# Kernel tuning notes

Measured on AMD Instinct MI355X. Metric: run time of the kernel, lower is better.

## Reference

```python
import jax, jax.numpy as jnp
import numpy as np

D_MODEL = 512
D_IN = D_MODEL * 2          # inner Mamba2 d_model
D_STATE = 128
D_CONV = 4
EXPAND = 2
D_INNER = EXPAND * D_IN     # 2048
HEADDIM = 64
NHEADS = D_INNER // HEADDIM # 32
CONV_DIM = D_INNER + 2 * D_STATE          # x,B,C stream into depthwise conv
D_PROJ = 2 * D_INNER + 2 * D_STATE + NHEADS  # z, xBC, dt
BATCH, SEQ = 2, 4096


def setup_inputs() -> dict:
    key = jax.random.key(0)
    ks = jax.random.split(key, 32)
    r = lambda i, shape, s=1.0: jax.random.normal(ks[i], shape, jnp.float32) * s
    inp = {"x": r(0, (BATCH, SEQ, D_MODEL))}
    inp.update(
        pre_w=r(1, (D_MODEL, D_IN), 0.02), pre_b=jnp.zeros(D_IN, jnp.float32),
        pre_ln_g=jnp.ones(D_IN, jnp.float32), pre_ln_b=jnp.zeros(D_IN, jnp.float32),
        post_w=r(2, (D_IN, D_MODEL), 0.02), post_b=jnp.zeros(D_MODEL, jnp.float32),
        post_ln_g=jnp.ones(D_MODEL, jnp.float32), post_ln_b=jnp.zeros(D_MODEL, jnp.float32),
    )
    for j, m in enumerate(("f", "b")):
        o = 3 + j * 8
        inp[f"win_{m}"] = r(o, (D_IN, D_PROJ), 0.02)
        inp[f"convw_{m}"] = r(o + 1, (CONV_DIM, D_CONV), 0.2)
        inp[f"convb_{m}"] = jnp.zeros(CONV_DIM, jnp.float32)
        inp[f"dtb_{m}"] = r(o + 2, (NHEADS,), 0.1)
        inp[f"Alog_{m}"] = jnp.log(jnp.arange(1, NHEADS + 1, dtype=jnp.float32))
        inp[f"D_{m}"] = jnp.ones(NHEADS, jnp.float32)
        inp[f"normw_{m}"] = jnp.ones(D_INNER, jnp.float32)
        inp[f"wout_{m}"] = r(o + 3, (D_INNER, D_IN), 0.02)
    return inp


def layernorm(x, g, b, eps=1e-5):
    mu = x.mean(-1, keepdims=True)
    v = ((x - mu) ** 2).mean(-1, keepdims=True)
    return (x - mu) * jax.lax.rsqrt(v + eps) * g + b


def dwconv_causal(x, w, b):
    # x: [B,L,C], w: [C,K] depthwise causal conv
    xp = jnp.pad(x, ((0, 0), (D_CONV - 1, 0), (0, 0)))
    y = jax.lax.conv_general_dilated(xp.transpose(0, 2, 1), w[:, None, :], (1,), 'VALID',
                                     feature_group_count=w.shape[0])
    return y.transpose(0, 2, 1) + b


def mamba2(x, win, convw, convb, dtb, Alog, Dp, normw, wout):
    # x: [B,L,D_IN]  ->  [B,L,D_IN]
    zxbcdt = x @ win
    z, xBC, dt = jnp.split(zxbcdt, [D_INNER, D_INNER + CONV_DIM], axis=-1)
    dt = jax.nn.softplus(dt + dtb)                          # [B,L,H]
    xBC = jax.nn.silu(dwconv_causal(xBC, convw, convb))
    xs, Bm, Cm = jnp.split(xBC, [D_INNER, D_INNER + D_STATE], axis=-1)
    xs = xs.reshape(xs.shape[0], xs.shape[1], NHEADS, HEADDIM)  # [B,L,H,P]
    A = -jnp.exp(Alog)                                       # [H]
    decay = jnp.exp(dt * A)                                  # [B,L,H]

    def step(h, inp):
        x_t, B_t, C_t, dt_t, dec_t = inp                     # [B,H,P],[B,N],[B,N],[B,H],[B,H]
        h = h * dec_t[:, :, None, None] + (dt_t[:, :, None] * x_t)[..., None] * B_t[:, None, None, :]
        y_t = jnp.einsum('bhpn,bn->bhp', h, C_t)
        return h, y_t

    h0 = jnp.zeros((x.shape[0], NHEADS, HEADDIM, D_STATE), x.dtype)
    seq = (xs.transpose(1, 0, 2, 3), Bm.transpose(1, 0, 2), Cm.transpose(1, 0, 2),
           dt.transpose(1, 0, 2), decay.transpose(1, 0, 2))
    _, ys = jax.lax.scan(step, h0, seq)                      # ys: [L,B,H,P]
    y = ys.transpose(1, 0, 2, 3) + Dp[None, None, :, None] * xs
    y = y.reshape(y.shape[0], y.shape[1], D_INNER)
    # gated RMSNorm (norm_before_gate=False)
    yg = y * jax.nn.silu(z)
    yn = yg * jax.lax.rsqrt(jnp.mean(yg * yg, -1, keepdims=True) + 1e-5) * normw
    return yn @ wout


def nbimamba2(x, pre_w, pre_b, pre_ln_g, pre_ln_b, post_w, post_b, post_ln_g, post_ln_b,
              win_f, convw_f, convb_f, dtb_f, Alog_f, D_f, normw_f, wout_f,
              win_b, convw_b, convb_b, dtb_b, Alog_b, D_b, normw_b, wout_b):
    shortcut = x
    h = layernorm(x @ pre_w + pre_b, pre_ln_g, pre_ln_b)
    gate = jax.nn.silu(h)
    out_f = mamba2(h, win_f, convw_f, convb_f, dtb_f, Alog_f, D_f, normw_f, wout_f)
    out_b = jnp.flip(mamba2(jnp.flip(h, 1), win_b, convw_b, convb_b, dtb_b, Alog_b, D_b, normw_b, wout_b), 1)
    out = layernorm((out_f * gate + out_b * gate) @ post_w + post_b, post_ln_g, post_ln_b)
    return out + shortcut


def reference(x, pre_w, pre_b, pre_ln_g, pre_ln_b, post_w, post_b, post_ln_g, post_ln_b,
              win_f, convw_f, convb_f, dtb_f, Alog_f, D_f, normw_f, wout_f,
              win_b, convw_b, convb_b, dtb_b, Alog_b, D_b, normw_b, wout_b):
    return nbimamba2(x, pre_w, pre_b, pre_ln_g, pre_ln_b, post_w, post_b, post_ln_g, post_ln_b,
                     win_f, convw_f, convb_f, dtb_f, Alog_f, D_f, normw_f, wout_f,
                     win_b, convw_b, convb_b, dtb_b, Alog_b, D_b, normw_b, wout_b)
```

## Files before the change

### kernel.cpp

```cpp
#include <hip/hip_runtime.h>
#include <stdint.h>

typedef unsigned short u16;
typedef __attribute__((ext_vector_type(8))) short short8;
typedef __attribute__((ext_vector_type(4))) float f32x4;

__device__ __forceinline__ float bf2f(u16 u) {
  union { float f; uint32_t i; } v; v.i = ((uint32_t)u) << 16; return v.f;
}
__device__ __forceinline__ u16 f2bf(float f) {
  union { float f; uint32_t i; } v; v.f = f;
  uint32_t r = v.i + 0x7FFFu + ((v.i >> 16) & 1u);
  return (u16)(r >> 16);
}
__device__ __forceinline__ uint32_t pk2(float a, float b) {
  return (uint32_t)f2bf(a) | ((uint32_t)f2bf(b) << 16);
}
__device__ __forceinline__ void gload16(const u16* g, u16* l) {
  __builtin_amdgcn_global_load_lds(
      (const __attribute__((address_space(1))) unsigned int*)g,
      (__attribute__((address_space(3))) unsigned int*)l, 16, 0, 0);
}

__device__ __forceinline__ float block_sum256(float v) {
  __shared__ float red[4];
  #pragma unroll
  for (int o = 1; o < 64; o <<= 1) v += __shfl_xor(v, o, 64);
  int lane = threadIdx.x & 63, w = threadIdx.x >> 6;
  __syncthreads();
  if (lane == 0) red[w] = v;
  __syncthreads();
  return red[0] + red[1] + red[2] + red[3];
}

__global__ void k_tcast(const float* __restrict__ W, u16* __restrict__ Wt,
                        int K, int N, int Npad) {
  __shared__ float tile[32][33];
  int n0 = blockIdx.x * 32, k0 = blockIdx.y * 32;
  int tx = threadIdx.x, ty0 = threadIdx.y;
  #pragma unroll
  for (int i = 0; i < 4; i++) {
    int ty = ty0 + i * 8;
    int k = k0 + ty, n = n0 + tx;
    tile[ty][tx] = (k < K && n < N) ? W[(size_t)k * N + n] : 0.f;
  }
  __syncthreads();
  #pragma unroll
  for (int i = 0; i < 4; i++) {
    int ty = ty0 + i * 8;
    int n = n0 + ty, k = k0 + tx;
    if (n < Npad && k < K) Wt[(size_t)n * K + k] = f2bf(tile[tx][ty]);
  }
}

__global__ void k_cast(const float* __restrict__ in, u16* __restrict__ out, int n4) {
  int i = blockIdx.x * 256 + threadIdx.x;
  if (i >= n4) return;
  float4 v = ((const float4*)in)[i];
  uint2 o;
  o.x = pk2(v.x, v.y);
  o.y = pk2(v.z, v.w);
  ((uint2*)out)[i] = o;
}

__launch_bounds__(256)
__global__ void k_gemm(const u16* __restrict__ A, const u16* __restrict__ Bt,
                       float* __restrict__ Cf, u16* __restrict__ Cb,
                       int M, int N, int K, int ldc, int flags) {
  __shared__ u16 lA[2][128 * 64];
  __shared__ u16 lB[2][128 * 64];
  const int tid = threadIdx.x;
  const int lane = tid & 63;
  const int wave = tid >> 6;
  const int bm = blockIdx.x, bn = blockIdx.y;
  const int wr = wave >> 1, wc = wave & 1;
  const int fr = lane & 15, fq = lane >> 4;

  const int srow = wave * 32 + (lane >> 3);
  const int scol = ((lane & 7) ^ (srow & 7)) * 8;
  const u16* gA = A + (size_t)(bm * 128 + srow) * K + scol;
  const u16* gB = Bt + (size_t)(bn * 128 + srow) * K + scol;
  const int lofs = wave * 2048;

  f32x4 acc[4][4] = {};

  #pragma unroll
  for (int i = 0; i < 4; i++) {
    gload16(gA + (size_t)(i * 8) * K, &lA[0][lofs + i * 512]);
    gload16(gB + (size_t)(i * 8) * K, &lB[0][lofs + i * 512]);
  }
  __syncthreads();

  const int NT = K >> 6;
  for (int t = 0; t < NT; ++t) {
    const int cur = t & 1;
    if (t + 1 < NT) {
      const int kt = (t + 1) << 6;
      #pragma unroll
      for (int i = 0; i < 4; i++) {
        gload16(gA + (size_t)(i * 8) * K + kt, &lA[cur ^ 1][lofs + i * 512]);
        gload16(gB + (size_t)(i * 8) * K + kt, &lB[cur ^ 1][lofs + i * 512]);
      }
    }
    #pragma unroll
    for (int kk = 0; kk < 2; kk++) {
      short8 af[4], bfr[4];
      #pragma unroll
      for (int m = 0; m < 4; m++) {
        int row = wr * 64 + m * 16 + fr;
        int sl = (kk * 4 + fq) ^ (row & 7);
        af[m] = *(const short8*)(&lA[cur][row * 64 + sl * 8]);
      }
      #pragma unroll
      for (int n = 0; n < 4; n++) {
        int row = wc * 64 + n * 16 + fr;
        int sl = (kk * 4 + fq) ^ (row & 7);
        bfr[n] = *(const short8*)(&lB[cur][row * 64 + sl * 8]);
      }
      #pragma unroll
      for (int m = 0; m < 4; m++)
        #pragma unroll
        for (int n = 0; n < 4; n++)
          acc[m][n] = __builtin_amdgcn_mfma_f32_16x16x32_bf16(af[m], bfr[n], acc[m][n], 0, 0, 0);
    }
    __syncthreads();
  }

  const bool bf16out = flags & 1, accum = flags & 2, flip = flags & 4;
  #pragma unroll
  for (int m = 0; m < 4; m++) {
    #pragma unroll
    for (int q = 0; q < 4; q++) {
      int rr = bm * 128 + wr * 64 + m * 16 + fq * 4 + q;
      int orow = flip ? (rr ^ 4095) : rr;
      size_t rb = (size_t)orow * ldc;
      #pragma unroll
      for (int n = 0; n < 4; n++) {
        int cc = bn * 128 + wc * 64 + n * 16 + fr;
        float v = acc[m][n][q];
        if (accum) v += Cf[rb + cc];
        if (bf16out) Cb[rb + cc] = f2bf(v);
        else Cf[rb + cc] = v;
      }
    }
  }
}

__global__ void k_preln(const float* __restrict__ t, const float* __restrict__ bias,
                        const float* __restrict__ g, const float* __restrict__ bb,
                        u16* __restrict__ out) {
  const int row = blockIdx.x, tid = threadIdx.x;
  float4 v = ((const float4*)(t + (size_t)row * 1024))[tid];
  float4 bi = ((const float4*)bias)[tid];
  float v0 = v.x + bi.x, v1 = v.y + bi.y, v2 = v.z + bi.z, v3 = v.w + bi.w;
  float mean = block_sum256(v0 + v1 + v2 + v3) * (1.f / 1024.f);
  float d0 = v0 - mean, d1 = v1 - mean, d2 = v2 - mean, d3 = v3 - mean;
  float var = block_sum256(d0 * d0 + d1 * d1 + d2 * d2 + d3 * d3) * (1.f / 1024.f);
  float rs = rsqrtf(var + 1e-5f);
  float4 gg = ((const float4*)g)[tid];
  float4 bv = ((const float4*)bb)[tid];
  uint2 o;
  o.x = pk2(d0 * rs * gg.x + bv.x, d1 * rs * gg.y + bv.y);
  o.y = pk2(d2 * rs * gg.z + bv.z, d3 * rs * gg.w + bv.w);
  ((uint2*)(out + (size_t)row * 1024))[tid] = o;
}

__global__ void k_dt2(const u16* __restrict__ zx, const float* __restrict__ dtb,
                      const float* __restrict__ Alog, float* __restrict__ DTt,
                      float* __restrict__ DECt, int flip) {
  int t = blockIdx.x * 256 + threadIdx.x;
  int h = blockIdx.y, b = blockIdx.z;
  int ts = flip ? 4095 - t : t;
  float raw = bf2f(zx[(size_t)((b << 12) + ts) * 4480 + 4352 + h]) + dtb[h];
  float d = (raw > 20.f) ? raw : log1pf(__expf(raw));
  size_t o = (size_t)(b * 32 + h) * 4096 + t;
  DTt[o] = d;
  DECt[o] = __expf(-__expf(Alog[h]) * d);
}

__global__ void k_conv2(const u16* __restrict__ zx, const float* __restrict__ cw,
                        const float* __restrict__ cb, u16* __restrict__ XT,
                        u16* __restrict__ BCtok, u16* __restrict__ BCT, int flip) {
  const int ct = blockIdx.x;
  const int tt = blockIdx.y;
  const int b = blockIdx.z;
  const int tid = threadIdx.x;
  __shared__ float sin_[67][64];
  __shared__ float sout[64][65];
  const int ch0 = ct * 64, t0 = tt * 64;

  for (int i = tid; i < 67 * 64; i += 256) {
    int r = i >> 6, ch = i & 63;
    int tok = t0 - 3 + r;
    float v = 0.f;
    if (tok >= 0) {
      int src = (b << 12) + (flip ? 4095 - tok : tok);
      v = bf2f(zx[(size_t)src * 4480 + 2048 + ch0 + ch]);
    }
    sin_[r][ch] = v;
  }
  __syncthreads();

  const int ch = tid & 63, g = tid >> 6;
  const int chg = ch0 + ch;
  float4 wv = *(const float4*)(cw + (size_t)chg * 4);
  float bias = cb[chg];
  #pragma unroll
  for (int i = 0; i < 16; i++) {
    int tl = g * 16 + i;
    float a = bias + wv.x * sin_[tl][ch] + wv.y * sin_[tl + 1][ch]
                   + wv.z * sin_[tl + 2][ch] + wv.w * sin_[tl + 3][ch];
    sout[tl][ch] = a / (1.f + __expf(-a));
  }
  __syncthreads();

  if (ch0 < 2048) {
    #pragma unroll
    for (int k = 0; k < 16; k++) {
      int chw = g + k * 4;
      int tl = tid & 63;
      XT[((size_t)(b * 2048 + ch0 + chw)) * 4096 + t0 + tl] = f2bf(sout[tl][chw]);
    }
  } else {
    int c2b = (ct - 32) * 64;
    #pragma unroll
    for (int k = 0; k < 16; k++) {
      int chw = g + k * 4;
      int tl = tid & 63;
      BCT[((size_t)(b * 256 + c2b + chw)) * 4096 + t0 + tl] = f2bf(sout[tl][chw]);
    }
    #pragma unroll
    for (int k = 0; k < 16; k++) {
      int r = g + k * 4;
      BCtok[((size_t)(b * 4096 + t0 + r)) * 256 + c2b + ch] = f2bf(sout[r][ch]);
    }
  }
}

#define NCH 16
#define SWZ(row, oct, msk) (((oct) ^ ((row) & (msk))) << 4)

__device__ __forceinline__ void cumsum256(int tid, int lane, float adt, float dtv,
                                          float* sL, float* sdt, float* spart) {
  float v = adt;
  if (tid < 256) {
    #pragma unroll
    for (int o = 1; o < 64; o <<= 1) {
      float t = __shfl_up(v, o, 64);
      if (lane >= o) v += t;
    }
    if (lane == 63) spart[tid >> 6] = v;
  }
  __syncthreads();
  if (tid < 256) {
    int w = tid >> 6;
    float off = 0.f;
    #pragma unroll
    for (int j = 0; j < 3; j++) if (j < w) off += spart[j];
    sL[tid] = v + off;
    sdt[tid] = dtv;
  }
}

__launch_bounds__(512, 1)
__global__ void k_ssd_a(const u16* __restrict__ XT, const u16* __restrict__ BCT,
                        const float* __restrict__ DTt, const float* __restrict__ Alog,
                        float* __restrict__ HB, float* __restrict__ PR) {
  const int c = blockIdx.x, h = blockIdx.y, b = blockIdx.z;
  const int tid = threadIdx.x;
  const int lane = tid & 63, w = tid >> 6;
  const int fr = lane & 15, fq = lane >> 4;
  const int bh = b * 32 + h;

  __shared__ u16 sX[64 * 256];
  __shared__ u16 sBW[128 * 256];
  __shared__ float sL[256], sdt[256], sw_[256], spart[4];

  float dtv = 0.f;
  if (tid < 256) dtv = DTt[(size_t)bh * 4096 + c * 256 + tid];
  float expA = __expf(Alog[h]);
  cumsum256(tid, lane, -expA * dtv, dtv, sL, sdt, spart);
  __syncthreads();
  if (tid < 256) sw_[tid] = __expf(sL[255] - sL[tid]) * sdt[tid];
  for (int i = tid; i < 2048; i += 512) {
    int p = i >> 5, oct = i & 31;
    uint4 v = *(const uint4*)(XT + ((size_t)(b * 2048 + h * 64 + p) << 12) + c * 256 + oct * 8);
    *(uint4*)((char*)sX + p * 512 + SWZ(p, oct, 15)) = v;
  }
  __syncthreads();
  for (int i = tid; i < 4096; i += 512) {
    int n = i >> 5, oct = i & 31;
    uint4 v = *(const uint4*)(BCT + ((size_t)(b * 256 + n) << 12) + c * 256 + oct * 8);
    const float* swp = sw_ + oct * 8;
    float f0 = bf2f((u16)(v.x & 0xFFFF)) * swp[0];
    float f1 = bf2f((u16)(v.x >> 16)) * swp[1];
    float f2 = bf2f((u16)(v.y & 0xFFFF)) * swp[2];
    float f3 = bf2f((u16)(v.y >> 16)) * swp[3];
    float f4 = bf2f((u16)(v.z & 0xFFFF)) * swp[4];
    float f5 = bf2f((u16)(v.z >> 16)) * swp[5];
    float f6 = bf2f((u16)(v.w & 0xFFFF)) * swp[6];
    float f7 = bf2f((u16)(v.w >> 16)) * swp[7];
    uint4 o;
    o.x = pk2(f0, f1); o.y = pk2(f2, f3); o.z = pk2(f4, f5); o.w = pk2(f6, f7);
    *(uint4*)((char*)sBW + n * 512 + SWZ(n, oct, 15)) = o;
  }
  __syncthreads();

  const int pb = w >> 1, nh = w & 1;
  f32x4 acc[4] = {};
  #pragma unroll
  for (int ks = 0; ks < 8; ks++) {
    int p = pb * 16 + fr;
    short8 af = *(const short8*)((char*)sX + p * 512 + SWZ(p, ks * 4 + fq, 15));
    #pragma unroll
    for (int nb = 0; nb < 4; nb++) {
      int n = nh * 64 + nb * 16 + fr;
      short8 bfm = *(const short8*)((char*)sBW + n * 512 + SWZ(n, ks * 4 + fq, 15));
      acc[nb] = __builtin_amdgcn_mfma_f32_16x16x32_bf16(af, bfm, acc[nb], 0, 0, 0);
    }
  }
  float* hb = HB + (size_t)(bh * NCH + c) * 8192;
  #pragma unroll
  for (int nb = 0; nb < 4; nb++)
    #pragma unroll
    for (int q = 0; q < 4; q++) {
      int p = pb * 16 + fq * 4 + q;
      int n = nh * 64 + nb * 16 + fr;
      hb[p * 128 + n] = acc[nb][q];
    }
  if (tid == 0) PR[bh * NCH + c] = __expf(sL[255]);
}

__global__ void k_scan_b(float* __restrict__ HB, const float* __restrict__ PR) {
  const int eb = blockIdx.x, h = blockIdx.y, b = blockIdx.z;
  const int e = eb * 256 + threadIdx.x;
  const int bh = b * 32 + h;
  float* base = HB + (size_t)bh * NCH * 8192 + e;
  const float* pr = PR + bh * NCH;
  float carry = 0.f;
  #pragma unroll 4
  for (int c = 0; c < NCH; ++c) {
    float v = base[(size_t)c * 8192];
    base[(size_t)c * 8192] = carry;
    carry = pr[c] * carry + v;
  }
}

__launch_bounds__(512, 1)
__global__ void k_ssd_c(const u16* __restrict__ BCtok, const u16* __restrict__ XT,
                        const float* __restrict__ DTt, const float* __restrict__ HB,
                        const float* __restrict__ Alog, const float* __restrict__ Dp,
                        u16* __restrict__ Y) {
  const int c = blockIdx.x, h = blockIdx.y, b = blockIdx.z;
  const int tid = threadIdx.x;
  const int lane = tid & 63, w = tid >> 6;
  const int fr = lane & 15, fq = lane >> 4;
  const int bh = b * 32 + h;
  const size_t m0 = (size_t)b * 4096 + c * 256;

  __shared__ u16 sB[256 * 128];
  __shared__ u16 sX[64 * 256];
  __shared__ u16 sH[64 * 128];
  __shared__ u16 sP[8 * 32 * 64];
  __shared__ float sL[256], sdt[256], spart[4];

  float dtv = 0.f;
  if (tid < 256) dtv = DTt[(size_t)bh * 4096 + c * 256 + tid];
  float expA = __expf(Alog[h]);
  cumsum256(tid, lane, -expA * dtv, dtv, sL, sdt, spart);

  for (int i = tid; i < 4096; i += 512) {
    int tr = i >> 4, oct = i & 15;
    uint4 v = *(const uint4*)(BCtok + ((m0 + tr) << 8) + oct * 8);
    *(uint4*)((char*)sB + tr * 256 + SWZ(tr, oct, 15)) = v;
  }
  for (int i = tid; i < 2048; i += 512) {
    int p = i >> 5, oct = i & 31;
    uint4 v = *(const uint4*)(XT + ((size_t)(b * 2048 + h * 64 + p) << 12) + c * 256 + oct * 8);
    *(uint4*)((char*)sX + p * 512 + SWZ(p, oct, 15)) = v;
  }
  for (int i = tid; i < 1024; i += 512) {
    int p = i >> 4, oct = i & 15;
    const float* src = HB + (size_t)(bh * NCH + c) * 8192 + p * 128 + oct * 8;
    float4 a = *(const float4*)src;
    float4 bb4 = *(const float4*)(src + 4);
    uint4 o;
    o.x = pk2(a.x, a.y); o.y = pk2(a.z, a.w); o.z = pk2(bb4.x, bb4.y); o.w = pk2(bb4.z, bb4.w);
    *(uint4*)((char*)sH + p * 256 + SWZ(p, oct, 15)) = o;
  }
  short8 cf[2][4];
  #pragma unroll
  for (int m = 0; m < 2; m++)
    #pragma unroll
    for (int ks = 0; ks < 4; ks++)
      cf[m][ks] = *(const short8*)(BCtok + ((m0 + w * 32 + m * 16 + fr) << 8) + 128 + ks * 32 + fq * 8);
  __syncthreads();

  float Lt[2][4], eLt[2][4];
  #pragma unroll
  for (int m = 0; m < 2; m++)
    #pragma unroll
    for (int q = 0; q < 4; q++) {
      Lt[m][q] = sL[w * 32 + m * 16 + fq * 4 + q];
      eLt[m][q] = __expf(Lt[m][q]);
    }
  const float Dh = Dp[h];

  f32x4 accY[2][4] = {};
  u16* pw = sP + w * 2048;
  const int ntl = (w >> 1) + 1;
  for (int tt = 0; tt < ntl; tt++) {
    const int t0 = tt * 64;
    f32x4 g[2][4] = {};
    #pragma unroll
    for (int ks = 0; ks < 4; ks++) {
      short8 bfm[4];
      #pragma unroll
      for (int nb = 0; nb < 4; nb++) {
        int tr = t0 + nb * 16 + fr;
        bfm[nb] = *(const short8*)((char*)sB + tr * 256 + SWZ(tr, ks * 4 + fq, 15));
      }
      #pragma unroll
      for (int m = 0; m < 2; m++)
        #pragma unroll
        for (int nb = 0; nb < 4; nb++)
          g[m][nb] = __builtin_amdgcn_mfma_f32_16x16x32_bf16(cf[m][ks], bfm[nb], g[m][nb], 0, 0, 0);
    }
    #pragma unroll
    for (int nb = 0; nb < 4; nb++) {
      int tau = t0 + nb * 16 + fr;
      float Ltau = sL[tau], dtau = sdt[tau];
      #pragma unroll
      for (int m = 0; m < 2; m++) {
        #pragma unroll
        for (int q = 0; q < 4; q++) {
          int t = w * 32 + m * 16 + fq * 4 + q;
          float mask = (tau > t) ? 0.f : __expf(Lt[m][q] - Ltau) * dtau;
          float pv = mask * g[m][nb][q];
          pv = (tau == t) ? pv + Dh : pv;
          int tl = m * 16 + fq * 4 + q, taul = nb * 16 + fr;
          *(u16*)((char*)pw + tl * 128 + ((((taul) >> 3) ^ (tl & 7)) << 4) + (taul & 7) * 2) = f2bf(pv);
        }
      }
    }
    #pragma unroll
    for (int ks = 0; ks < 2; ks++) {
      short8 pf[2], xf[4];
      #pragma unroll
      for (int m = 0; m < 2; m++) {
        int tl = m * 16 + fr;
        pf[m] = *(const short8*)((char*)pw + tl * 128 + (((ks * 4 + fq) ^ (tl & 7)) << 4));
      }
      #pragma unroll
      for (int pb = 0; pb < 4; pb++) {
        int p = pb * 16 + fr;
        int oct = (t0 >> 3) + ks * 4 + fq;
        xf[pb] = *(const short8*)((char*)sX + p * 512 + SWZ(p, oct, 15));
      }
      #pragma unroll
      for (int m = 0; m < 2; m++)
        #pragma unroll
        for (int pb = 0; pb < 4; pb++)
          accY[m][pb] = __builtin_amdgcn_mfma_f32_16x16x32_bf16(pf[m], xf[pb], accY[m][pb], 0, 0, 0);
    }
  }
  f32x4 accO[2][4] = {};
  #pragma unroll
  for (int ks = 0; ks < 4; ks++) {
    short8 hf[4];
    #pragma unroll
    for (int pb = 0; pb < 4; pb++) {
      int p = pb * 16 + fr;
      hf[pb] = *(const short8*)((char*)sH + p * 256 + SWZ(p, ks * 4 + fq, 15));
    }
    #pragma unroll
    for (int m = 0; m < 2; m++)
      #pragma unroll
      for (int pb = 0; pb < 4; pb++)
        accO[m][pb] = __builtin_amdgcn_mfma_f32_16x16x32_bf16(cf[m][ks], hf[pb], accO[m][pb], 0, 0, 0);
  }
  #pragma unroll
  for (int m = 0; m < 2; m++)
    #pragma unroll
    for (int pb = 0; pb < 4; pb++)
      #pragma unroll
      for (int q = 0; q < 4; q++) {
        int t = w * 32 + m * 16 + fq * 4 + q;
        float val = accY[m][pb][q] + eLt[m][q] * accO[m][pb][q];
        Y[(m0 + t) * 2048 + h * 64 + pb * 16 + fr] = f2bf(val);
      }
}

__launch_bounds__(256)
__global__ void k_scan(const u16* __restrict__ XT, const u16* __restrict__ BCtok,
                       const float* __restrict__ DTt, const float* __restrict__ DECt,
                       const float* __restrict__ Dp, u16* __restrict__ y) {
  const int ps = blockIdx.x, h = blockIdx.y, b = blockIdx.z;
  const int tid = threadIdx.x;
  const int tsub = tid & 15, pl = tid >> 4;
  const int p = ps * 16 + pl;
  const u16* xp = XT + ((size_t)(b * 2048 + h * 64 + p)) * 4096;
  const float* dth = DTt + (size_t)(b * 32 + h) * 4096;
  const float* dch = DECt + (size_t)(b * 32 + h) * 4096;
  u16* yp = y + (size_t)b * 4096 * 2048 + h * 64 + p;
  const float Dh = Dp[h];
  float s0 = 0, s1 = 0, s2 = 0, s3 = 0, s4 = 0, s5 = 0, s6 = 0, s7 = 0;
  for (int tau = 0; tau < 4096; ++tau) {
    const u16* bcr = BCtok + ((size_t)(b * 4096 + tau)) * 256;
    uint4 vB = *(const uint4*)(bcr + tsub * 8);
    uint4 vC = *(const uint4*)(bcr + 128 + tsub * 8);
    float xv = bf2f(xp[tau]);
    float a = dth[tau] * xv;
    float dcv = dch[tau];
    s0 = s0 * dcv + a * bf2f((u16)(vB.x & 0xFFFF)); s1 = s1 * dcv + a * bf2f((u16)(vB.x >> 16));
    s2 = s2 * dcv + a * bf2f((u16)(vB.y & 0xFFFF)); s3 = s3 * dcv + a * bf2f((u16)(vB.y >> 16));
    s4 = s4 * dcv + a * bf2f((u16)(vB.z & 0xFFFF)); s5 = s5 * dcv + a * bf2f((u16)(vB.z >> 16));
    s6 = s6 * dcv + a * bf2f((u16)(vB.w & 0xFFFF)); s7 = s7 * dcv + a * bf2f((u16)(vB.w >> 16));
    float sum = s0 * bf2f((u16)(vC.x & 0xFFFF)) + s1 * bf2f((u16)(vC.x >> 16))
              + s2 * bf2f((u16)(vC.y & 0xFFFF)) + s3 * bf2f((u16)(vC.y >> 16))
              + s4 * bf2f((u16)(vC.z & 0xFFFF)) + s5 * bf2f((u16)(vC.z >> 16))
              + s6 * bf2f((u16)(vC.w & 0xFFFF)) + s7 * bf2f((u16)(vC.w >> 16));
    sum += __shfl_xor(sum, 1, 64);
    sum += __shfl_xor(sum, 2, 64);
    sum += __shfl_xor(sum, 4, 64);
    sum += __shfl_xor(sum, 8, 64);
    if (tsub == 0) yp[(size_t)tau * 2048] = f2bf(sum + Dh * xv);
  }
}

__global__ void k_gate(const u16* __restrict__ y, const u16* __restrict__ zx,
                       const float* __restrict__ normw, u16* __restrict__ u, int flip) {
  const int m = blockIdx.x, tid = threadIdx.x;
  const int ms = flip ? (m ^ 4095) : m;
  const u16* yr = y + (size_t)m * 2048;
  const u16* zr = zx + (size_t)ms * 4480;
  float vals[8];
  float ss = 0.f;
  #pragma unroll
  for (int i = 0; i < 8; i++) {
    int c = i * 256 + tid;
    float zv = bf2f(zr[c]);
    float wv = bf2f(yr[c]) * (zv / (1.f + __expf(-zv)));
    vals[i] = wv;
    ss += wv * wv;
  }
  float rs = rsqrtf(block_sum256(ss) * (1.f / 2048.f) + 1e-5f);
  #pragma unroll
  for (int i = 0; i < 8; i++) {
    int c = i * 256 + tid;
    u[(size_t)m * 2048 + c] = f2bf(vals[i] * rs * normw[c]);
  }
}

__global__ void k_u2(const float* __restrict__ s, const u16* __restrict__ hpre,
                     u16* __restrict__ u2) {
  int i = blockIdx.x * 256 + threadIdx.x;
  float hv = bf2f(hpre[i]);
  u2[i] = f2bf(s[i] * (hv / (1.f + __expf(-hv))));
}

__global__ void k_final(const float* __restrict__ t2, const float* __restrict__ bias,
                        const float* __restrict__ g, const float* __restrict__ bb,
                        const float* __restrict__ x, float* __restrict__ out) {
  const int row = blockIdx.x, tid = threadIdx.x;
  float2 v = ((const float2*)(t2 + (size_t)row * 512))[tid];
  float v0 = v.x + bias[tid * 2], v1 = v.y + bias[tid * 2 + 1];
  float mean = block_sum256(v0 + v1) * (1.f / 512.f);
  float d0 = v0 - mean, d1 = v1 - mean;
  float var = block_sum256(d0 * d0 + d1 * d1) * (1.f / 512.f);
  float rs = rsqrtf(var + 1e-5f);
  float2 xr = ((const float2*)(x + (size_t)row * 512))[tid];
  float2 o;
  o.x = d0 * rs * g[tid * 2] + bb[tid * 2] + xr.x;
  o.y = d1 * rs * g[tid * 2 + 1] + bb[tid * 2 + 1] + xr.y;
  ((float2*)(out + (size_t)row * 512))[tid] = o;
}

extern "C" void kernel_launch(void* const* d_in, const int* in_sizes, int n_in,
                              void* d_out, int out_size, void* d_ws, size_t ws_size,
                              hipStream_t stream) {
  const float* x      = (const float*)d_in[0];
  const float* pre_w  = (const float*)d_in[1];
  const float* pre_b  = (const float*)d_in[2];
  const float* pre_g  = (const float*)d_in[3];
  const float* pre_bb = (const float*)d_in[4];
  const float* post_w = (const float*)d_in[5];
  const float* post_b = (const float*)d_in[6];
  const float* post_g = (const float*)d_in[7];
  const float* post_bb= (const float*)d_in[8];
  const float* win_[2]   = {(const float*)d_in[9],  (const float*)d_in[17]};
  const float* convw_[2] = {(const float*)d_in[10], (const float*)d_in[18]};
  const float* convb_[2] = {(const float*)d_in[11], (const float*)d_in[19]};
  const float* dtb_[2]   = {(const float*)d_in[12], (const float*)d_in[20]};
  const float* Alog_[2]  = {(const float*)d_in[13], (const float*)d_in[21]};
  const float* Dp_[2]    = {(const float*)d_in[14], (const float*)d_in[22]};
  const float* normw_[2] = {(const float*)d_in[15], (const float*)d_in[23]};
  const float* wout_[2]  = {(const float*)d_in[16], (const float*)d_in[24]};

  char* ws = (char*)d_ws;
  constexpr size_t OFF_WT_PRE  = 0;
  constexpr size_t OFF_WT_WINF = OFF_WT_PRE  + 1048576;
  constexpr size_t OFF_WT_WINB = OFF_WT_WINF + 9175040;
  constexpr size_t OFF_WT_WOF  = OFF_WT_WINB + 9175040;
  constexpr size_t OFF_WT_WOB  = OFF_WT_WOF  + 4194304;
  constexpr size_t OFF_WT_POST = OFF_WT_WOB  + 4194304;
  constexpr size_t OFF_HPRE    = OFF_WT_POST + 1048576;
  constexpr size_t OFF_ZX      = OFF_HPRE + 16777216;
  constexpr size_t OFF_XT      = OFF_ZX + 73400320;
  constexpr size_t OFF_BC      = OFF_XT + 33554432;
  constexpr size_t OFF_DT      = OFF_BC + 8388608;
  constexpr size_t OFF_DEC     = OFF_DT + 1048576;
  constexpr size_t OFF_Y       = OFF_DEC + 1048576;
  constexpr size_t OFF_S       = OFF_Y + 33554432;
  constexpr size_t OFF_HB      = OFF_S + 33554432;
  constexpr size_t ARENA_END   = OFF_HB + 33554432;

  u16* WtPre    = (u16*)(ws + OFF_WT_PRE);
  u16* WtWin[2] = {(u16*)(ws + OFF_WT_WINF), (u16*)(ws + OFF_WT_WINB)};
  u16* WtWo[2]  = {(u16*)(ws + OFF_WT_WOF),  (u16*)(ws + OFF_WT_WOB)};
  u16* WtPost   = (u16*)(ws + OFF_WT_POST);
  u16* HPRE = (u16*)(ws + OFF_HPRE);
  u16* ZX   = (u16*)(ws + OFF_ZX);
  u16* XT   = (u16*)(ws + OFF_XT);
  u16* BCtok= (u16*)(ws + OFF_BC);
  u16* BCT  = (u16*)(ws + OFF_BC + 4194304);
  float* DTt = (float*)(ws + OFF_DT);
  float* DECt= (float*)(ws + OFF_DEC);
  u16*  Y   = (u16*)(ws + OFF_Y);
  float* S  = (float*)(ws + OFF_S);
  float* HB = (float*)(ws + OFF_HB);
  float* PRb  = (float*)(ws + OFF_WT_PRE);
  u16*   XBF  = (u16*)(ws + OFF_Y);
  float* TMP  = S;
  u16*   U    = (u16*)(ws + OFF_XT);
  u16*   U2   = ZX;
  float* TMP2 = (float*)(ws + OFF_XT);

  const bool chunked = (ws_size >= ARENA_END);

  dim3 tb(32, 8);
  k_tcast<<<dim3(32, 16),  tb, 0, stream>>>(pre_w,   WtPre,    512, 1024, 1024);
  k_tcast<<<dim3(140, 32), tb, 0, stream>>>(win_[0], WtWin[0], 1024, 4384, 4480);
  k_tcast<<<dim3(140, 32), tb, 0, stream>>>(win_[1], WtWin[1], 1024, 4384, 4480);
  k_tcast<<<dim3(32, 64),  tb, 0, stream>>>(wout_[0], WtWo[0], 2048, 1024, 1024);
  k_tcast<<<dim3(32, 64),  tb, 0, stream>>>(wout_[1], WtWo[1], 2048, 1024, 1024);
  k_tcast<<<dim3(16, 32),  tb, 0, stream>>>(post_w,  WtPost,   1024,  512,  512);
  k_cast<<<4096, 256, 0, stream>>>(x, XBF, 1048576);
  k_gemm<<<dim3(64, 8), 256, 0, stream>>>(XBF, WtPre, TMP, nullptr, 8192, 1024, 512, 1024, 0);
  k_preln<<<8192, 256, 0, stream>>>(TMP, pre_b, pre_g, pre_bb, HPRE);

  for (int d = 0; d < 2; d++) {
    int flip = d;
    k_gemm<<<dim3(64, 35), 256, 0, stream>>>(HPRE, WtWin[d], nullptr, ZX, 8192, 4480, 1024, 4480, 1);
    k_dt2<<<dim3(16, 32, 2), 256, 0, stream>>>(ZX, dtb_[d], Alog_[d], DTt, DECt, flip);
    k_conv2<<<dim3(36, 64, 2), 256, 0, stream>>>(ZX, convw_[d], convb_[d], XT, BCtok, BCT, flip);
    if (chunked) {
      k_ssd_a<<<dim3(NCH, 32, 2), 512, 0, stream>>>(XT, BCT, DTt, Alog_[d], HB, PRb);
      k_scan_b<<<dim3(32, 32, 2), 256, 0, stream>>>(HB, PRb);
      k_ssd_c<<<dim3(NCH, 32, 2), 512, 0, stream>>>(BCtok, XT, DTt, HB, Alog_[d], Dp_[d], Y);
    } else {
      k_scan<<<dim3(4, 32, 2), 256, 0, stream>>>(XT, BCtok, DTt, DECt, Dp_[d], Y);
    }
    k_gate<<<8192, 256, 0, stream>>>(Y, ZX, normw_[d], U, flip);
    k_gemm<<<dim3(64, 8), 256, 0, stream>>>(U, WtWo[d], S, nullptr, 8192, 1024, 2048, 1024,
                                            d ? (2 | 4) : 0);
  }

  k_u2<<<32768, 256, 0, stream>>>(S, HPRE, U2);
  k_gemm<<<dim3(64, 4), 256, 0, stream>>>(U2, WtPost, TMP2, nullptr, 8192, 512, 1024, 512, 0);
  k_final<<<8192, 256, 0, stream>>>(TMP2, post_b, post_g, post_bb, x, (float*)d_out);
}
```

Before: 770.7 us.

## Add 256x256-tile double-buffered GEMM for the in-projection

Adds a dedicated 512-thread GEMM kernel with 256x256 output tiles, double-buffered LDS staging via global_load_lds, XOR-swizzled shared layout and setprio around MFMA bursts. It is used for the large in-projection GEMM (8192x4480x1024) in both directions in place of the generic 128x128 kernel. The aim is more data reuse per loaded tile and overlap of loads with compute. In exchange it uses 128KB of LDS (one block per CU) and launches only 576 blocks, which can leave the machine unevenly loaded. It also wastes work on the clamped last N tile, since 4480 is not a multiple of 256.

Measured after the change: 805.8 us. 4.6% more time.

```diff
diff --git a/kernel.cpp b/kernel.cpp
--- a/kernel.cpp
+++ b/kernel.cpp
@@ -141,6 +141,103 @@
         if (accum) v += Cf[rb + cc];
         if (bf16out) Cb[rb + cc] = f2bf(v);
         else Cf[rb + cc] = v;
+      }
+    }
+  }
+}
+
+__launch_bounds__(512)
+__global__ void k_gemm256(const u16* __restrict__ A, const u16* __restrict__ Bt,
+                          u16* __restrict__ Cb) {
+  constexpr int K = 1024, N = 4480, NT = 16;
+  __shared__ u16 lA[2][256 * 64];
+  __shared__ u16 lB[2][256 * 64];
+  const int tid = threadIdx.x;
+  const int lane = tid & 63;
+  const int wid = tid >> 6;
+  const int bm = blockIdx.x, bn = blockIdx.y;
+  const int wr = wid >> 2, wc = wid & 3;
+  const int fr = lane & 15, fq = lane >> 4;
+
+  const int srow = tid >> 3;
+  const int scol = ((tid & 7) ^ (srow & 7)) * 8;
+  const u16* gA[4];
+  const u16* gB[4];
+  #pragma unroll
+  for (int i = 0; i < 4; i++) {
+    int arow = bm * 256 + i * 64 + srow;
+    gA[i] = A + (size_t)arow * K + scol;
+    int brow = bn * 256 + i * 64 + srow;
+    if (brow > N - 1) brow = N - 1;
+    gB[i] = Bt + (size_t)brow * K + scol;
+  }
+
+  f32x4 acc[8][4] = {};
+
+  auto stage_all = [&](int u) {
+    if (u >= NT) return;
+    const int buf = u & 1, kt = u << 6;
+    #pragma unroll
+    for (int i = 0; i < 4; i++)
+      gload16(gA[i] + kt, &lA[buf][i * 4096 + tid * 8]);
+    #pragma unroll
+    for (int i = 0; i < 4; i++)
+      gload16(gB[i] + kt, &lB[buf][i * 4096 + tid * 8]);
+  };
+
+  stage_all(0);
+  stage_all(1);
+  asm volatile("s_waitcnt vmcnt(8)" ::: "memory");
+  __builtin_amdgcn_s_barrier();
+
+  for (int t = 0; t < NT; ++t) {
+    const u16* bufA = &lA[t & 1][0];
+    const u16* bufB = &lB[t & 1][0];
+    #pragma unroll
+    for (int p = 0; p < 4; p++) {
+      const int mh = p >> 1, kk = p & 1;
+      short8 af[4], bfm[4];
+      #pragma unroll
+      for (int j = 0; j < 4; j++) {
+        int row = wr * 128 + (mh * 4 + j) * 16 + fr;
+        int sl = (kk * 4 + fq) ^ (row & 7);
+        af[j] = *(const short8*)(&bufA[row * 64 + sl * 8]);
+      }
+      #pragma unroll
+      for (int n = 0; n < 4; n++) {
+        int row = wc * 64 + n * 16 + fr;
+        int sl = (kk * 4 + fq) ^ (row & 7);
+        bfm[n] = *(const short8*)(&bufB[row * 64 + sl * 8]);
+      }
+      __builtin_amdgcn_s_barrier();
+      __builtin_amdgcn_s_setprio(1);
+      #pragma unroll
+      for (int j = 0; j < 4; j++)
+        #pragma unroll
+        for (int n = 0; n < 4; n++)
+          acc[mh * 4 + j][n] =
+              __builtin_amdgcn_mfma_f32_16x16x32_bf16(af[j], bfm[n], acc[mh * 4 + j][n], 0, 0, 0);
+      __builtin_amdgcn_s_setprio(0);
+      __builtin_amdgcn_s_barrier();
+    }
+    stage_all(t + 2);
+    if (t + 2 < NT) {
+      asm volatile("s_waitcnt vmcnt(8)" ::: "memory");
+    } else {
+      asm volatile("s_waitcnt vmcnt(0)" ::: "memory");
+    }
+    __builtin_amdgcn_s_barrier();
+  }
+
+  #pragma unroll
+  for (int m = 0; m < 8; m++) {
+    #pragma unroll
+    for (int q = 0; q < 4; q++) {
+      size_t rb = (size_t)(bm * 256 + wr * 128 + m * 16 + fq * 4 + q) * N;
+      #pragma unroll
+      for (int n = 0; n < 4; n++) {
+        int cc = bn * 256 + wc * 64 + n * 16 + fr;
+        if (cc < N) Cb[rb + cc] = f2bf(acc[m][n][q]);
       }
     }
   }
@@ -651,7 +748,7 @@
 
   for (int d = 0; d < 2; d++) {
     int flip = d;
-    k_gemm<<<dim3(64, 35), 256, 0, stream>>>(HPRE, WtWin[d], nullptr, ZX, 8192, 4480, 1024, 4480, 1);
+    k_gemm256<<<dim3(32, 18), 512, 0, stream>>>(HPRE, WtWin[d], ZX);
     k_dt2<<<dim3(16, 32, 2), 256, 0, stream>>>(ZX, dtb_[d], Alog_[d], DTt, DECt, flip);
     k_conv2<<<dim3(36, 64, 2), 256, 0, stream>>>(ZX, convw_[d], convb_[d], XT, BCtok, BCT, flip);
     if (chunked) {
```
